# Performance work log

Measured on AMD Instinct MI355X. Metric: run time of the kernel, lower is better.

## Reference

```python
import jax, jax.numpy as jnp
import numpy as np

N_NODES = 50000
N_EDGES = 800000
D_IN = 16


def gcn_conv(x, edge_index, W, b, n_nodes):
    """PyG GCNConv: x' = D^{-1/2} (A + I) D^{-1/2} X W + b (add_self_loops=True)."""
    h = x @ W  # [N, d_out] - transform before propagate (small d => cheaper)
    src = jnp.concatenate([edge_index[0], jnp.arange(n_nodes)])  # add self-loops
    dst = jnp.concatenate([edge_index[1], jnp.arange(n_nodes)])
    deg = jax.ops.segment_sum(jnp.ones_like(dst, dtype=h.dtype), dst,
                              num_segments=n_nodes)  # in-degree incl. self-loop
    deg_inv_sqrt = jnp.where(deg > 0, jax.lax.rsqrt(deg), 0.0)
    norm = deg_inv_sqrt[src] * deg_inv_sqrt[dst]  # [E+N]
    msg = h[src] * norm[:, None]                  # gather + scale
    out = jax.ops.segment_sum(msg, dst, num_segments=n_nodes)  # scatter-add
    return out + b


def setup_inputs() -> dict:
    key = jax.random.key(0)
    ks = jax.random.split(key, 16)
    d = D_IN
    x = jax.random.normal(ks[0], (N_NODES, d), dtype=jnp.float32)
    edge_index = jax.random.randint(ks[1], (2, N_EDGES), 0, N_NODES, dtype=jnp.int64)

    def glorot(k, fan_in, fan_out):
        s = (6.0 / (fan_in + fan_out)) ** 0.5
        return jax.random.uniform(k, (fan_in, fan_out), jnp.float32, -s, s)

    return {
        "x": x,
        "edge_index": edge_index,
        "W1": glorot(ks[2], d, 2 * d),      "b1": jnp.zeros((2 * d,), jnp.float32),
        "W2": glorot(ks[3], 2 * d, 4 * d),  "b2": jnp.zeros((4 * d,), jnp.float32),
        "W3": glorot(ks[4], 4 * d, 8 * d),  "b3": jnp.zeros((8 * d,), jnp.float32),
        "Wl1": glorot(ks[5], 8 * d, 4 * d), "bl1": jnp.zeros((4 * d,), jnp.float32),
        "Wl2": glorot(ks[6], 4 * d, 2 * d), "bl2": jnp.zeros((2 * d,), jnp.float32),
        "Wl3": glorot(ks[7], 2 * d, d),     "bl3": jnp.zeros((d,), jnp.float32),
    }


def reference(x, edge_index, W1, b1, W2, b2, W3, b3, Wl1, bl1, Wl2, bl2, Wl3, bl3):
    n = x.shape[0]
    # note: original applies relu twice per conv; relu is idempotent
    out = jax.nn.relu(gcn_conv(x, edge_index, W1, b1, n))
    out = jax.nn.relu(gcn_conv(out, edge_index, W2, b2, n))
    out = jax.nn.relu(gcn_conv(out, edge_index, W3, b3, n))
    out = jax.nn.relu(out @ Wl1 + bl1)
    out = jax.nn.relu(out @ Wl2 + bl2)
    out = jax.nn.relu(out @ Wl3 + bl3)
    return out
```

## Files before the change

kernel.cpp:

```cpp
#include <hip/hip_runtime.h>

#define TPB 256
#define TE  2048
#define MAXB 6144

typedef _Float16 half_t;
typedef _Float16 half4 __attribute__((ext_vector_type(4)));
typedef _Float16 half8 __attribute__((ext_vector_type(8)));
typedef float float8v __attribute__((ext_vector_type(8)));
typedef float f32x4 __attribute__((ext_vector_type(4)));

static inline int cdiv(int a, int b) { return (a + b - 1) / b; }


__global__ void __launch_bounds__(TPB)
k_binscatter(const int* __restrict__ src, const int* __restrict__ dst,
             int* __restrict__ bcur, int* __restrict__ ncnt,
             unsigned int* __restrict__ gbuf, int e, int nb) {
    __shared__ int lcnt[256], loffs[256], lcur[256], gres[256];
    __shared__ int ss[256];
    __shared__ unsigned int ldata[TE];
    const int tid = threadIdx.x;
    const int base = blockIdx.x * TE;
    const int cnt = min(TE, e - base);
    lcnt[tid] = 0;
    __syncthreads();

    unsigned int myv[TE / TPB];
    int myb[TE / TPB];
#pragma unroll
    for (int k = 0; k < TE / TPB; ++k) {
        int j = tid + k * TPB;
        if (j < cnt) {
            int d = dst[base + j], s = src[base + j];
            int b = d >> 8;
            myv[k] = ((unsigned)b << 24) | ((unsigned)(d & 255) << 16) | (unsigned)s;
            myb[k] = b;
            atomicAdd(&lcnt[b], 1);
            atomicAdd(&ncnt[d], 1);
        } else myb[k] = -1;
    }
    __syncthreads();
    {
        int v = lcnt[tid];
        ss[tid] = v;
        __syncthreads();
        for (int d = 1; d < 256; d <<= 1) {
            int x2 = (tid >= d) ? ss[tid - d] : 0;
            __syncthreads();
            ss[tid] += x2;
            __syncthreads();
        }
        loffs[tid] = ss[tid] - v;
        lcur[tid] = ss[tid] - v;
    }
    __syncthreads();
    if (tid < nb && lcnt[tid])
        gres[tid] = tid * MAXB + atomicAdd(&bcur[tid], lcnt[tid]);
#pragma unroll
    for (int k = 0; k < TE / TPB; ++k) {
        if (myb[k] >= 0) {
            int p = atomicAdd(&lcur[myb[k]], 1);
            ldata[p] = myv[k];
        }
    }
    __syncthreads();
    for (int j = tid; j < cnt; j += TPB) {
        unsigned int v = ldata[j];
        int b = v >> 24;
        gbuf[gres[b] + (j - loffs[b])] = v & 0xFFFFFFu;
    }
}

__global__ void __launch_bounds__(TPB)
k_csr(const unsigned int* __restrict__ gbuf, const int* __restrict__ bcur,
      const int* __restrict__ ncnt, const float* __restrict__ x,
      int* __restrict__ offs, unsigned short* __restrict__ nch,
      float* __restrict__ dinv, unsigned short* __restrict__ ssrc,
      half_t* __restrict__ G, int n, int nb) {
    __shared__ int ss[256], lcur2[256];
    __shared__ float sdinv[256];
    __shared__ unsigned short stage[MAXB];
    const int b = blockIdx.x;
    const int t = threadIdx.x;
    const int s0 = b * MAXB;
    const int m = bcur[b];

    const int v = ncnt[b * 256 + t];
    const int pv = (v + 7) & ~7;
    ss[t] = pv;
    __syncthreads();
    for (int d = 1; d < 256; d <<= 1) {
        int x2 = (t >= d) ? ss[t - d] : 0;
        __syncthreads();
        ss[t] += x2;
        __syncthreads();
    }
    const int lo = ss[t] - pv;
    lcur2[t] = lo;
    float di = rsqrtf((float)v + 1.0f);
    sdinv[t] = di;
    int node = b * 256 + t;
    if (node < n) {
        offs[node] = s0 + lo;
        nch[node] = (unsigned short)(pv >> 3);
        dinv[node] = di;
    }
    __syncthreads();
    for (int j = t; j < m; j += TPB) {
        unsigned int u = gbuf[s0 + j];
        int p = atomicAdd(&lcur2[(u >> 16) & 255], 1);
        stage[p] = (unsigned short)(u & 0xFFFFu);
    }
    __syncthreads();
    for (int q = lo + v; q < lo + pv; ++q)
        stage[q] = (unsigned short)n;
    __syncthreads();
    const int tot = ss[255];
    for (int j = t; j < tot; j += TPB) ssrc[s0 + j] = stage[j];

    const int base = b * 256;
    const int cn = min(256, n - base);
    const float4* X4 = (const float4*)x;
    half4* G4 = (half4*)G;
    for (int j = t; j < cn * 4; j += TPB) {
        int nl = j >> 2, k4 = j & 3;
        float4 vv = X4[(size_t)(base + nl) * 4 + k4];
        float d = sdinv[nl];
        half4 h;
        h.x = (half_t)(vv.x * d); h.y = (half_t)(vv.y * d);
        h.z = (half_t)(vv.z * d); h.w = (half_t)(vv.w * d);
        G4[(size_t)(base + nl) * 4 + k4] = h;
    }
    if (b == 0 && t < 4) G4[(size_t)n * 4 + t] = half4{0, 0, 0, 0};
}

template<int DI, int DO, int R, bool SCALE, bool OUT_HALF, bool WHALF, bool ZSENT>
__global__ void __launch_bounds__(TPB, 4)
k_conv(const int* __restrict__ offs, const unsigned short* __restrict__ nch,
       const unsigned short* __restrict__ ssrc,
       const half_t* __restrict__ G, const float* __restrict__ dinv,
       const float* __restrict__ W, const float* __restrict__ b,
       void* __restrict__ outp, int n) {
    constexpr int CT = DO / 4;
    constexpr int RT = TPB / CT;
    constexpr int TM = RT * R;
    constexpr int K4 = DI / 4;
    constexpr int PX = K4 + 1;
    constexpr int C  = DI / 8;
    static_assert(TM * C == TPB, "gather/gemm tile mismatch");
    __shared__ float4 sW4[WHALF ? 1 : DI * CT];
    __shared__ half4  sWh[WHALF ? DI * CT : 1];
    __shared__ float4 sX4[TM * PX];
    __shared__ int soffs[TM];
    __shared__ unsigned short snch[TM];
    const int tid = threadIdx.x;
    const int r0 = blockIdx.x * TM;

    const float4* Wg = (const float4*)W;
    for (int t = tid; t < DI * CT; t += TPB) {
        float4 w = Wg[t];
        if (WHALF) {
            half4 h;
            h.x = (half_t)w.x; h.y = (half_t)w.y;
            h.z = (half_t)w.z; h.w = (half_t)w.w;
            sWh[t] = h;
        } else {
            sW4[t] = w;
        }
    }
    if (tid < TM) {
        int row = r0 + tid;
        soffs[tid] = (row < n) ? offs[row] : 0;
        snch[tid] = (row < n) ? nch[row] : (unsigned short)0;
    }
    __syncthreads();

    {
        int lrow = tid / C;
        int gc = tid - lrow * C;
        int row = r0 + lrow;
        float8v acc;
#pragma unroll
        for (int q = 0; q < 8; ++q) acc[q] = 0.f;
        if (row < n) {
            const half8* Grow = (const half8*)G;
            const unsigned gcU = (unsigned)gc;
            half8 hs = Grow[(unsigned)row * C + gcU];
#pragma unroll
            for (int q = 0; q < 8; ++q) acc[q] = (float)hs[q];
            const int nchunks = snch[lrow];
            const uint4* sv = (const uint4*)(ssrc + soffs[lrow]);
            int k = 0;
            for (; k + 2 <= nchunks; k += 2) {
                uint4 pa = sv[k];
                uint4 pb = sv[k + 1];
                unsigned a0 = pa.x & 0xFFFFu, a1 = pa.x >> 16;
                unsigned a2 = pa.y & 0xFFFFu, a3 = pa.y >> 16;
                unsigned a4 = pa.z & 0xFFFFu, a5 = pa.z >> 16;
                unsigned a6 = pa.w & 0xFFFFu, a7 = pa.w >> 16;
                unsigned b0 = pb.x & 0xFFFFu, b1 = pb.x >> 16;
                unsigned b2 = pb.y & 0xFFFFu, b3 = pb.y >> 16;
                unsigned b4 = pb.z & 0xFFFFu, b5 = pb.z >> 16;
                unsigned b6 = pb.w & 0xFFFFu, b7 = pb.w >> 16;
                half8 ga0 = Grow[a0 * C + gcU];
                half8 ga1 = Grow[a1 * C + gcU];
                half8 ga2 = Grow[a2 * C + gcU];
                half8 ga3 = Grow[a3 * C + gcU];
                half8 ga4 = Grow[a4 * C + gcU];
                half8 ga5 = Grow[a5 * C + gcU];
                half8 ga6 = Grow[a6 * C + gcU];
                half8 ga7 = Grow[a7 * C + gcU];
                half8 gb0 = Grow[b0 * C + gcU];
                half8 gb1 = Grow[b1 * C + gcU];
                half8 gb2 = Grow[b2 * C + gcU];
                half8 gb3 = Grow[b3 * C + gcU];
                half8 gb4 = Grow[b4 * C + gcU];
                half8 gb5 = Grow[b5 * C + gcU];
                half8 gb6 = Grow[b6 * C + gcU];
                half8 gb7 = Grow[b7 * C + gcU];
#pragma unroll
                for (int q = 0; q < 8; ++q)
                    acc[q] += (((((float)ga0[q] + (float)ga1[q]) + ((float)ga2[q] + (float)ga3[q]))
                             +  (((float)ga4[q] + (float)ga5[q]) + ((float)ga6[q] + (float)ga7[q])))
                             + ((((float)gb0[q] + (float)gb1[q]) + ((float)gb2[q] + (float)gb3[q]))
                             +  (((float)gb4[q] + (float)gb5[q]) + ((float)gb6[q] + (float)gb7[q]))));
            }
            if (k < nchunks) {
                uint4 pk = sv[k];
                unsigned a0 = pk.x & 0xFFFFu, a1 = pk.x >> 16;
                unsigned a2 = pk.y & 0xFFFFu, a3 = pk.y >> 16;
                unsigned a4 = pk.z & 0xFFFFu, a5 = pk.z >> 16;
                unsigned a6 = pk.w & 0xFFFFu, a7 = pk.w >> 16;
                half8 g0 = Grow[a0 * C + gcU];
                half8 g1 = Grow[a1 * C + gcU];
                half8 g2 = Grow[a2 * C + gcU];
                half8 g3 = Grow[a3 * C + gcU];
                half8 g4 = Grow[a4 * C + gcU];
                half8 g5 = Grow[a5 * C + gcU];
                half8 g6 = Grow[a6 * C + gcU];
                half8 g7 = Grow[a7 * C + gcU];
#pragma unroll
                for (int q = 0; q < 8; ++q)
                    acc[q] += (((float)g0[q] + (float)g1[q]) + ((float)g2[q] + (float)g3[q]))
                            + (((float)g4[q] + (float)g5[q]) + ((float)g6[q] + (float)g7[q]));
            }
            float di = dinv[row];
#pragma unroll
            for (int q = 0; q < 8; ++q) acc[q] *= di;
        }
        sX4[lrow * PX + 2 * gc]     = make_float4(acc[0], acc[1], acc[2], acc[3]);
        sX4[lrow * PX + 2 * gc + 1] = make_float4(acc[4], acc[5], acc[6], acc[7]);
    }
    __syncthreads();

    const int c = tid & (CT - 1);
    const int rg = tid / CT;
    const int rbase = rg * R;
    float4 acc[R];
#pragma unroll
    for (int r = 0; r < R; ++r) acc[r] = make_float4(0.f, 0.f, 0.f, 0.f);
#pragma unroll 2
    for (int k4 = 0; k4 < K4; ++k4) {
        float4 xv[R];
#pragma unroll
        for (int r = 0; r < R; ++r) xv[r] = sX4[(rbase + r) * PX + k4];
#pragma unroll
        for (int kk = 0; kk < 4; ++kk) {
            float4 wv;
            if (WHALF) {
                half4 wh = sWh[(k4 * 4 + kk) * CT + c];
                wv = make_float4((float)wh.x, (float)wh.y, (float)wh.z, (float)wh.w);
            } else {
                wv = sW4[(k4 * 4 + kk) * CT + c];
            }
#pragma unroll
            for (int r = 0; r < R; ++r) {
                float xs = (kk == 0) ? xv[r].x : (kk == 1) ? xv[r].y
                         : (kk == 2) ? xv[r].z : xv[r].w;
                acc[r].x += xs * wv.x; acc[r].y += xs * wv.y;
                acc[r].z += xs * wv.z; acc[r].w += xs * wv.w;
            }
        }
    }

    float4 bc = ((const float4*)b)[c];
#pragma unroll
    for (int r = 0; r < R; ++r) {
        int row = r0 + rbase + r;
        if (row < n) {
            float4 o;
            o.x = fmaxf(acc[r].x + bc.x, 0.f);
            o.y = fmaxf(acc[r].y + bc.y, 0.f);
            o.z = fmaxf(acc[r].z + bc.z, 0.f);
            o.w = fmaxf(acc[r].w + bc.w, 0.f);
            if (SCALE) {
                float d = dinv[row];
                o.x *= d; o.y *= d; o.z *= d; o.w *= d;
            }
            if (OUT_HALF) {
                half4 h;
                h.x = (half_t)o.x; h.y = (half_t)o.y;
                h.z = (half_t)o.z; h.w = (half_t)o.w;
                ((half4*)outp)[(size_t)row * CT + c] = h;
            } else {
                ((float4*)outp)[(size_t)row * CT + c] = o;
            }
        }
    }
    if (ZSENT && OUT_HALF && blockIdx.x == 0 && tid < CT)
        ((half4*)outp)[(size_t)n * CT + tid] = half4{0, 0, 0, 0};
}

__global__ void __launch_bounds__(TPB, 4)
k_conv3_head(const int* __restrict__ offs, const unsigned short* __restrict__ nch,
             const unsigned short* __restrict__ ssrc,
             const half_t* __restrict__ G, const float* __restrict__ dinv,
             const float* __restrict__ W, const float* __restrict__ b,
             const float* __restrict__ Wl1, const float* __restrict__ bl1,
             const float* __restrict__ Wl2, const float* __restrict__ bl2,
             const float* __restrict__ Wl3, const float* __restrict__ bl3,
             float* __restrict__ out, int n) {
    constexpr int TM = 32;
    constexpr int C  = 8;
    constexpr int XPA = 72;
    constexpr int XPB = 136;
    __shared__ __align__(16) union {
        struct { half_t sWhT[128 * XPA]; half_t X16[TM * XPA]; } g;
        struct { half_t X3[TM * XPB]; half_t sW1T[64 * XPB];
                 float h1[TM * 65]; float h2[TM * 33]; } h;
    } S;
    __shared__ int soffs[TM];
    __shared__ unsigned short snch[TM];
    const int tid = threadIdx.x;
    const int r0 = blockIdx.x * TM;
    const int lane = tid & 63;
    const int wv = tid >> 6;
    const int lr = lane & 15;
    const int kq = lane >> 4;

    {
        const float4* Wg = (const float4*)W;
        for (int t = tid; t < 64 * 32; t += TPB) {
            int k = t >> 5, c4 = t & 31;
            float4 w = Wg[t];
            S.g.sWhT[(c4 * 4 + 0) * XPA + k] = (half_t)w.x;
            S.g.sWhT[(c4 * 4 + 1) * XPA + k] = (half_t)w.y;
            S.g.sWhT[(c4 * 4 + 2) * XPA + k] = (half_t)w.z;
            S.g.sWhT[(c4 * 4 + 3) * XPA + k] = (half_t)w.w;
        }
    }
    if (tid < TM) {
        int row = r0 + tid;
        soffs[tid] = (row < n) ? offs[row] : 0;
        snch[tid] = (row < n) ? nch[row] : (unsigned short)0;
    }
    __syncthreads();

    {
        int lrow = tid / C;
        int gc = tid - lrow * C;
        int row = r0 + lrow;
        float8v acc;
#pragma unroll
        for (int q = 0; q < 8; ++q) acc[q] = 0.f;
        if (row < n) {
            const half8* Grow = (const half8*)G;
            const unsigned gcU = (unsigned)gc;
            half8 hs = Grow[(unsigned)row * C + gcU];
#pragma unroll
            for (int q = 0; q < 8; ++q) acc[q] = (float)hs[q];
            const int nchunks = snch[lrow];
            const uint4* sv = (const uint4*)(ssrc + soffs[lrow]);
            int k = 0;
            for (; k + 2 <= nchunks; k += 2) {
                uint4 pa = sv[k];
                uint4 pb = sv[k + 1];
                unsigned a0 = pa.x & 0xFFFFu, a1 = pa.x >> 16;
                unsigned a2 = pa.y & 0xFFFFu, a3 = pa.y >> 16;
                unsigned a4 = pa.z & 0xFFFFu, a5 = pa.z >> 16;
                unsigned a6 = pa.w & 0xFFFFu, a7 = pa.w >> 16;
                unsigned b0 = pb.x & 0xFFFFu, b1 = pb.x >> 16;
                unsigned b2 = pb.y & 0xFFFFu, b3 = pb.y >> 16;
                unsigned b4 = pb.z & 0xFFFFu, b5 = pb.z >> 16;
                unsigned b6 = pb.w & 0xFFFFu, b7 = pb.w >> 16;
                half8 ga0 = Grow[a0 * C + gcU];
                half8 ga1 = Grow[a1 * C + gcU];
                half8 ga2 = Grow[a2 * C + gcU];
                half8 ga3 = Grow[a3 * C + gcU];
                half8 ga4 = Grow[a4 * C + gcU];
                half8 ga5 = Grow[a5 * C + gcU];
                half8 ga6 = Grow[a6 * C + gcU];
                half8 ga7 = Grow[a7 * C + gcU];
                half8 gb0 = Grow[b0 * C + gcU];
                half8 gb1 = Grow[b1 * C + gcU];
                half8 gb2 = Grow[b2 * C + gcU];
                half8 gb3 = Grow[b3 * C + gcU];
                half8 gb4 = Grow[b4 * C + gcU];
                half8 gb5 = Grow[b5 * C + gcU];
                half8 gb6 = Grow[b6 * C + gcU];
                half8 gb7 = Grow[b7 * C + gcU];
#pragma unroll
                for (int q = 0; q < 8; ++q)
                    acc[q] += (((((float)ga0[q] + (float)ga1[q]) + ((float)ga2[q] + (float)ga3[q]))
                             +  (((float)ga4[q] + (float)ga5[q]) + ((float)ga6[q] + (float)ga7[q])))
                             + ((((float)gb0[q] + (float)gb1[q]) + ((float)gb2[q] + (float)gb3[q]))
                             +  (((float)gb4[q] + (float)gb5[q]) + ((float)gb6[q] + (float)gb7[q]))));
            }
            if (k < nchunks) {
                uint4 pk = sv[k];
                unsigned a0 = pk.x & 0xFFFFu, a1 = pk.x >> 16;
                unsigned a2 = pk.y & 0xFFFFu, a3 = pk.y >> 16;
                unsigned a4 = pk.z & 0xFFFFu, a5 = pk.z >> 16;
                unsigned a6 = pk.w & 0xFFFFu, a7 = pk.w >> 16;
                half8 g0 = Grow[a0 * C + gcU];
                half8 g1 = Grow[a1 * C + gcU];
                half8 g2 = Grow[a2 * C + gcU];
                half8 g3 = Grow[a3 * C + gcU];
                half8 g4 = Grow[a4 * C + gcU];
                half8 g5 = Grow[a5 * C + gcU];
                half8 g6 = Grow[a6 * C + gcU];
                half8 g7 = Grow[a7 * C + gcU];
#pragma unroll
                for (int q = 0; q < 8; ++q)
                    acc[q] += (((float)g0[q] + (float)g1[q]) + ((float)g2[q] + (float)g3[q]))
                            + (((float)g4[q] + (float)g5[q]) + ((float)g6[q] + (float)g7[q]));
            }
            float di = dinv[row];
#pragma unroll
            for (int q = 0; q < 8; ++q) acc[q] *= di;
        }
        half8 hv;
#pragma unroll
        for (int q = 0; q < 8; ++q) hv[q] = (half_t)acc[q];
        *(half8*)&S.g.X16[lrow * XPA + gc * 8] = hv;
    }
    __syncthreads();

    f32x4 acc3[2][2];
#pragma unroll
    for (int mt = 0; mt < 2; ++mt)
#pragma unroll
        for (int nt = 0; nt < 2; ++nt) acc3[mt][nt] = f32x4{0.f, 0.f, 0.f, 0.f};
#pragma unroll
    for (int ks = 0; ks < 2; ++ks) {
        half8 a0 = *(const half8*)&S.g.X16[lr * XPA + ks * 32 + kq * 8];
        half8 a1 = *(const half8*)&S.g.X16[(lr + 16) * XPA + ks * 32 + kq * 8];
        half8 b0 = *(const half8*)&S.g.sWhT[(wv * 32 + lr) * XPA + ks * 32 + kq * 8];
        half8 b1 = *(const half8*)&S.g.sWhT[(wv * 32 + 16 + lr) * XPA + ks * 32 + kq * 8];
        acc3[0][0] = __builtin_amdgcn_mfma_f32_16x16x32_f16(a0, b0, acc3[0][0], 0, 0, 0);
        acc3[0][1] = __builtin_amdgcn_mfma_f32_16x16x32_f16(a0, b1, acc3[0][1], 0, 0, 0);
        acc3[1][0] = __builtin_amdgcn_mfma_f32_16x16x32_f16(a1, b0, acc3[1][0], 0, 0, 0);
        acc3[1][1] = __builtin_amdgcn_mfma_f32_16x16x32_f16(a1, b1, acc3[1][1], 0, 0, 0);
    }
    const float bc30 = b[wv * 32 + lr];
    const float bc31 = b[wv * 32 + 16 + lr];
    __syncthreads();

#pragma unroll
    for (int mt = 0; mt < 2; ++mt)
#pragma unroll
        for (int nt = 0; nt < 2; ++nt) {
            float bb = nt ? bc31 : bc30;
#pragma unroll
            for (int j = 0; j < 4; ++j) {
                float v = fmaxf(acc3[mt][nt][j] + bb, 0.f);
                S.h.X3[(mt * 16 + kq * 4 + j) * XPB + wv * 32 + nt * 16 + lr] = (half_t)v;
            }
        }
    {
        const float4* W1g = (const float4*)Wl1;
        for (int t = tid; t < 128 * 16; t += TPB) {
            int k = t >> 4, c4 = t & 15;
            float4 w = W1g[t];
            S.h.sW1T[(c4 * 4 + 0) * XPB + k] = (half_t)w.x;
            S.h.sW1T[(c4 * 4 + 1) * XPB + k] = (half_t)w.y;
            S.h.sW1T[(c4 * 4 + 2) * XPB + k] = (half_t)w.z;
            S.h.sW1T[(c4 * 4 + 3) * XPB + k] = (half_t)w.w;
        }
    }
    __syncthreads();

    f32x4 h1a[2];
    h1a[0] = f32x4{0.f, 0.f, 0.f, 0.f};
    h1a[1] = f32x4{0.f, 0.f, 0.f, 0.f};
#pragma unroll
    for (int ks = 0; ks < 4; ++ks) {
        half8 a0 = *(const half8*)&S.h.X3[lr * XPB + ks * 32 + kq * 8];
        half8 a1 = *(const half8*)&S.h.X3[(lr + 16) * XPB + ks * 32 + kq * 8];
        half8 bb = *(const half8*)&S.h.sW1T[(wv * 16 + lr) * XPB + ks * 32 + kq * 8];
        h1a[0] = __builtin_amdgcn_mfma_f32_16x16x32_f16(a0, bb, h1a[0], 0, 0, 0);
        h1a[1] = __builtin_amdgcn_mfma_f32_16x16x32_f16(a1, bb, h1a[1], 0, 0, 0);
    }
    {
        float bb = bl1[wv * 16 + lr];
#pragma unroll
        for (int mt = 0; mt < 2; ++mt)
#pragma unroll
            for (int j = 0; j < 4; ++j)
                S.h.h1[(mt * 16 + kq * 4 + j) * 65 + wv * 16 + lr] =
                    fmaxf(h1a[mt][j] + bb, 0.f);
    }
    __syncthreads();

    {
        const int c4 = tid & 7;
        const int rl = tid >> 3;
        float a2[4] = {0.f, 0.f, 0.f, 0.f};
#pragma unroll 4
        for (int k = 0; k < 64; ++k) {
            float4 w = ((const float4*)Wl2)[k * 8 + c4];
            float xs = S.h.h1[rl * 65 + k];
            a2[0] += xs * w.x; a2[1] += xs * w.y;
            a2[2] += xs * w.z; a2[3] += xs * w.w;
        }
        float4 bc = ((const float4*)bl2)[c4];
        S.h.h2[rl * 33 + c4 * 4 + 0] = fmaxf(a2[0] + bc.x, 0.f);
        S.h.h2[rl * 33 + c4 * 4 + 1] = fmaxf(a2[1] + bc.y, 0.f);
        S.h.h2[rl * 33 + c4 * 4 + 2] = fmaxf(a2[2] + bc.z, 0.f);
        S.h.h2[rl * 33 + c4 * 4 + 3] = fmaxf(a2[3] + bc.w, 0.f);
    }
    __syncthreads();

    {
        const int c4 = tid & 3;
        const int rl = tid >> 2;
        if (rl < TM) {
            float s0 = 0.f, s1 = 0.f, s2 = 0.f, s3 = 0.f;
#pragma unroll 4
            for (int k = 0; k < 32; ++k) {
                float4 w = ((const float4*)Wl3)[k * 4 + c4];
                float xs = S.h.h2[rl * 33 + k];
                s0 += xs * w.x; s1 += xs * w.y;
                s2 += xs * w.z; s3 += xs * w.w;
            }
            int row = r0 + rl;
            if (row < n) {
                float4 bc = ((const float4*)bl3)[c4];
                float4 o;
                o.x = fmaxf(s0 + bc.x, 0.f);
                o.y = fmaxf(s1 + bc.y, 0.f);
                o.z = fmaxf(s2 + bc.z, 0.f);
                o.w = fmaxf(s3 + bc.w, 0.f);
                ((float4*)out)[(size_t)row * 4 + c4] = o;
            }
        }
    }
}

extern "C" void kernel_launch(void* const* d_in, const int* in_sizes, int n_in,
                              void* d_out, int out_size, void* d_ws, size_t ws_size,
                              hipStream_t stream) {
    const float* x   = (const float*)d_in[0];
    const int*   ei  = (const int*)d_in[1];
    const float* W1  = (const float*)d_in[2];
    const float* bb1 = (const float*)d_in[3];
    const float* W2  = (const float*)d_in[4];
    const float* bb2 = (const float*)d_in[5];
    const float* W3  = (const float*)d_in[6];
    const float* bb3 = (const float*)d_in[7];
    const float* Wl1 = (const float*)d_in[8];
    const float* bl1 = (const float*)d_in[9];
    const float* Wl2 = (const float*)d_in[10];
    const float* bl2 = (const float*)d_in[11];
    const float* Wl3 = (const float*)d_in[12];
    const float* bl3 = (const float*)d_in[13];
    float* out = (float*)d_out;

    const int n = in_sizes[0] / 16;
    const int e = in_sizes[1] / 2;
    const int* src = ei;
    const int* dst = ei + e;
    const int nb = cdiv(n, 256);

    char* p = (char*)d_ws;
    auto alloc = [&](size_t bytes) {
        char* r = p;
        p += (bytes + 255) & ~(size_t)255;
        return r;
    };
    int*            bcur = (int*)           alloc(1024);
    int*            ncnt = (int*)           alloc((size_t)nb * 256 * 4);
    float*          dinv = (float*)         alloc((size_t)n * 4);
    int*            offs = (int*)           alloc((size_t)n * 4);
    unsigned short* nch  = (unsigned short*)alloc((size_t)n * 2);
    unsigned int*   gbuf = (unsigned int*)  alloc((size_t)nb * MAXB * 4);
    unsigned short* ssrc = (unsigned short*)alloc((size_t)nb * MAXB * 2);
    half_t*         H1   = (half_t*)        alloc((size_t)(n + 1) * 64 * 2);
    half_t*         H2   = (half_t*)        alloc((size_t)(n + 1) * 32 * 2);

    hipMemsetAsync(bcur, 0, 1024 + (size_t)nb * 256 * 4, stream);
    k_binscatter<<<cdiv(e, TE), TPB, 0, stream>>>(src, dst, bcur, ncnt, gbuf, e, nb);
    k_csr<<<nb, TPB, 0, stream>>>(gbuf, bcur, ncnt, x, offs, nch, dinv, ssrc, H1, n, nb);

    k_conv<16, 32, 4, true, true, false, true><<<cdiv(n, 128), TPB, 0, stream>>>(
        offs, nch, ssrc, H1, dinv, W1, bb1, H2, n);
    k_conv<32, 64, 4, true, true, false, true><<<cdiv(n, 64), TPB, 0, stream>>>(
        offs, nch, ssrc, H2, dinv, W2, bb2, H1, n);
    k_conv3_head<<<cdiv(n, 32), TPB, 0, stream>>>(
        offs, nch, ssrc, H1, dinv, W3, bb3, Wl1, bl1, Wl2, bl2, Wl3, bl3, out, n);
}
```

Before: 204.3 us.

## Pretranspose head weights to fp16 globally and sort CSR neighbor lists

Adds a small prep kernel that converts W3 and Wl1 to transposed fp16 layouts once per call. The fused conv3+head kernel then reads MFMA B operands straight from global/L2 instead of staging and transposing weights into shared memory in every block. This shrinks LDS use, and the launch-bounds occupancy hint rises from 4 to 6. Separately, each node's neighbor list in the CSR build is insertion-sorted by source index to improve gather locality, at the cost of extra serial work per thread in k_csr.

```diff
diff --git a/kernel.cpp b/kernel.cpp
--- a/kernel.cpp
+++ b/kernel.cpp
@@ -12,6 +12,29 @@
 
 static inline int cdiv(int a, int b) { return (a + b - 1) / b; }
 
+
+__global__ void __launch_bounds__(TPB)
+k_wprep(const float* __restrict__ W3, const float* __restrict__ Wl1,
+        half_t* __restrict__ w3t, half_t* __restrict__ w1t) {
+    const int tid = threadIdx.x;
+    if (blockIdx.x == 0) {
+        for (int t = tid; t < 128 * 16; t += TPB) {
+            int c = t >> 4, k4 = t & 15;
+            half4 h;
+#pragma unroll
+            for (int i = 0; i < 4; ++i) h[i] = (half_t)W3[(k4 * 4 + i) * 128 + c];
+            *(half4*)&w3t[c * 64 + k4 * 4] = h;
+        }
+    } else {
+        for (int t = tid; t < 64 * 32; t += TPB) {
+            int c = t >> 5, k4 = t & 31;
+            half4 h;
+#pragma unroll
+            for (int i = 0; i < 4; ++i) h[i] = (half_t)Wl1[(k4 * 4 + i) * 64 + c];
+            *(half4*)&w1t[c * 128 + k4 * 4] = h;
+        }
+    }
+}
 
 __global__ void __launch_bounds__(TPB)
 k_binscatter(const int* __restrict__ src, const int* __restrict__ dst,
@@ -113,8 +136,16 @@
         stage[p] = (unsigned short)(u & 0xFFFFu);
     }
     __syncthreads();
-    for (int q = lo + v; q < lo + pv; ++q)
-        stage[q] = (unsigned short)n;
+    {
+        for (int q = lo + 1; q < lo + v; ++q) {
+            unsigned short key = stage[q];
+            int w = q - 1;
+            while (w >= lo && stage[w] > key) { stage[w + 1] = stage[w]; --w; }
+            stage[w + 1] = key;
+        }
+        for (int q = lo + v; q < lo + pv; ++q)
+            stage[q] = (unsigned short)n;
+    }
     __syncthreads();
     const int tot = ss[255];
     for (int j = t; j < tot; j += TPB) ssrc[s0 + j] = stage[j];
@@ -312,12 +343,12 @@
         ((half4*)outp)[(size_t)n * CT + tid] = half4{0, 0, 0, 0};
 }
 
-__global__ void __launch_bounds__(TPB, 4)
+__global__ void __launch_bounds__(TPB, 6)
 k_conv3_head(const int* __restrict__ offs, const unsigned short* __restrict__ nch,
              const unsigned short* __restrict__ ssrc,
              const half_t* __restrict__ G, const float* __restrict__ dinv,
-             const float* __restrict__ W, const float* __restrict__ b,
-             const float* __restrict__ Wl1, const float* __restrict__ bl1,
+             const half_t* __restrict__ w3t, const float* __restrict__ b,
+             const half_t* __restrict__ w1t, const float* __restrict__ bl1,
              const float* __restrict__ Wl2, const float* __restrict__ bl2,
              const float* __restrict__ Wl3, const float* __restrict__ bl3,
              float* __restrict__ out, int n) {
@@ -326,9 +357,8 @@
     constexpr int XPA = 72;
     constexpr int XPB = 136;
     __shared__ __align__(16) union {
-        struct { half_t sWhT[128 * XPA]; half_t X16[TM * XPA]; } g;
-        struct { half_t X3[TM * XPB]; half_t sW1T[64 * XPB];
-                 float h1[TM * 65]; float h2[TM * 33]; } h;
+        struct { half_t X16[TM * XPA]; } g;
+        struct { half_t X3[TM * XPB]; float h1[TM * 65]; float h2[TM * 33]; } h;
     } S;
     __shared__ int soffs[TM];
     __shared__ unsigned short snch[TM];
@@ -339,17 +369,6 @@
     const int lr = lane & 15;
     const int kq = lane >> 4;
 
-    {
-        const float4* Wg = (const float4*)W;
-        for (int t = tid; t < 64 * 32; t += TPB) {
-            int k = t >> 5, c4 = t & 31;
-            float4 w = Wg[t];
-            S.g.sWhT[(c4 * 4 + 0) * XPA + k] = (half_t)w.x;
-            S.g.sWhT[(c4 * 4 + 1) * XPA + k] = (half_t)w.y;
-            S.g.sWhT[(c4 * 4 + 2) * XPA + k] = (half_t)w.z;
-            S.g.sWhT[(c4 * 4 + 3) * XPA + k] = (half_t)w.w;
-        }
-    }
     if (tid < TM) {
         int row = r0 + tid;
         soffs[tid] = (row < n) ? offs[row] : 0;
@@ -442,16 +461,19 @@
     for (int mt = 0; mt < 2; ++mt)
 #pragma unroll
         for (int nt = 0; nt < 2; ++nt) acc3[mt][nt] = f32x4{0.f, 0.f, 0.f, 0.f};
-#pragma unroll
-    for (int ks = 0; ks < 2; ++ks) {
-        half8 a0 = *(const half8*)&S.g.X16[lr * XPA + ks * 32 + kq * 8];
-        half8 a1 = *(const half8*)&S.g.X16[(lr + 16) * XPA + ks * 32 + kq * 8];
-        half8 b0 = *(const half8*)&S.g.sWhT[(wv * 32 + lr) * XPA + ks * 32 + kq * 8];
-        half8 b1 = *(const half8*)&S.g.sWhT[(wv * 32 + 16 + lr) * XPA + ks * 32 + kq * 8];
-        acc3[0][0] = __builtin_amdgcn_mfma_f32_16x16x32_f16(a0, b0, acc3[0][0], 0, 0, 0);
-        acc3[0][1] = __builtin_amdgcn_mfma_f32_16x16x32_f16(a0, b1, acc3[0][1], 0, 0, 0);
-        acc3[1][0] = __builtin_amdgcn_mfma_f32_16x16x32_f16(a1, b0, acc3[1][0], 0, 0, 0);
-        acc3[1][1] = __builtin_amdgcn_mfma_f32_16x16x32_f16(a1, b1, acc3[1][1], 0, 0, 0);
+    {
+        const half8* W3r = (const half8*)w3t;
+#pragma unroll
+        for (int ks = 0; ks < 2; ++ks) {
+            half8 a0 = *(const half8*)&S.g.X16[lr * XPA + ks * 32 + kq * 8];
+            half8 a1 = *(const half8*)&S.g.X16[(lr + 16) * XPA + ks * 32 + kq * 8];
+            half8 b0 = W3r[(wv * 32 + lr) * 8 + ks * 4 + kq];
+            half8 b1 = W3r[(wv * 32 + 16 + lr) * 8 + ks * 4 + kq];
+            acc3[0][0] = __builtin_amdgcn_mfma_f32_16x16x32_f16(a0, b0, acc3[0][0], 0, 0, 0);
+            acc3[0][1] = __builtin_amdgcn_mfma_f32_16x16x32_f16(a0, b1, acc3[0][1], 0, 0, 0);
+            acc3[1][0] = __builtin_amdgcn_mfma_f32_16x16x32_f16(a1, b0, acc3[1][0], 0, 0, 0);
+            acc3[1][1] = __builtin_amdgcn_mfma_f32_16x16x32_f16(a1, b1, acc3[1][1], 0, 0, 0);
+        }
     }
     const float bc30 = b[wv * 32 + lr];
     const float bc31 = b[wv * 32 + 16 + lr];
@@ -468,29 +490,21 @@
                 S.h.X3[(mt * 16 + kq * 4 + j) * XPB + wv * 32 + nt * 16 + lr] = (half_t)v;
             }
         }
-    {
-        const float4* W1g = (const float4*)Wl1;
-        for (int t = tid; t < 128 * 16; t += TPB) {
-            int k = t >> 4, c4 = t & 15;
-            float4 w = W1g[t];
-            S.h.sW1T[(c4 * 4 + 0) * XPB + k] = (half_t)w.x;
-            S.h.sW1T[(c4 * 4 + 1) * XPB + k] = (half_t)w.y;
-            S.h.sW1T[(c4 * 4 + 2) * XPB + k] = (half_t)w.z;
-            S.h.sW1T[(c4 * 4 + 3) * XPB + k] = (half_t)w.w;
-        }
-    }
     __syncthreads();
 
     f32x4 h1a[2];
     h1a[0] = f32x4{0.f, 0.f, 0.f, 0.f};
     h1a[1] = f32x4{0.f, 0.f, 0.f, 0.f};
-#pragma unroll
-    for (int ks = 0; ks < 4; ++ks) {
-        half8 a0 = *(const half8*)&S.h.X3[lr * XPB + ks * 32 + kq * 8];
-        half8 a1 = *(const half8*)&S.h.X3[(lr + 16) * XPB + ks * 32 + kq * 8];
-        half8 bb = *(const half8*)&S.h.sW1T[(wv * 16 + lr) * XPB + ks * 32 + kq * 8];
-        h1a[0] = __builtin_amdgcn_mfma_f32_16x16x32_f16(a0, bb, h1a[0], 0, 0, 0);
-        h1a[1] = __builtin_amdgcn_mfma_f32_16x16x32_f16(a1, bb, h1a[1], 0, 0, 0);
+    {
+        const half8* W1r = (const half8*)w1t;
+#pragma unroll
+        for (int ks = 0; ks < 4; ++ks) {
+            half8 a0 = *(const half8*)&S.h.X3[lr * XPB + ks * 32 + kq * 8];
+            half8 a1 = *(const half8*)&S.h.X3[(lr + 16) * XPB + ks * 32 + kq * 8];
+            half8 bb = W1r[(wv * 16 + lr) * 16 + ks * 4 + kq];
+            h1a[0] = __builtin_amdgcn_mfma_f32_16x16x32_f16(a0, bb, h1a[0], 0, 0, 0);
+            h1a[1] = __builtin_amdgcn_mfma_f32_16x16x32_f16(a1, bb, h1a[1], 0, 0, 0);
+        }
     }
     {
         float bb = bl1[wv * 16 + lr];
@@ -588,8 +602,11 @@
     unsigned short* ssrc = (unsigned short*)alloc((size_t)nb * MAXB * 2);
     half_t*         H1   = (half_t*)        alloc((size_t)(n + 1) * 64 * 2);
     half_t*         H2   = (half_t*)        alloc((size_t)(n + 1) * 32 * 2);
+    half_t*         w3t  = (half_t*)        alloc(128 * 64 * 2);
+    half_t*         w1t  = (half_t*)        alloc(64 * 128 * 2);
 
     hipMemsetAsync(bcur, 0, 1024 + (size_t)nb * 256 * 4, stream);
+    k_wprep<<<2, TPB, 0, stream>>>(W3, Wl1, w3t, w1t);
     k_binscatter<<<cdiv(e, TE), TPB, 0, stream>>>(src, dst, bcur, ncnt, gbuf, e, nb);
     k_csr<<<nb, TPB, 0, stream>>>(gbuf, bcur, ncnt, x, offs, nch, dinv, ssrc, H1, n, nb);
 
@@ -598,5 +615,5 @@
     k_conv<32, 64, 4, true, true, false, true><<<cdiv(n, 64), TPB, 0, stream>>>(
         offs, nch, ssrc, H2, dinv, W2, bb2, H1, n);
     k_conv3_head<<<cdiv(n, 32), TPB, 0, stream>>>(
-        offs, nch, ssrc, H1, dinv, W3, bb3, Wl1, bl1, Wl2, bl2, Wl3, bl3, out, n);
+        offs, nch, ssrc, H1, dinv, w3t, bb3, w1t, bl1, Wl2, bl2, Wl3, bl3, out, n);
 }
```

New measurement: 272.3 us. 33.3% more time.
